# Optimization experiments

Hardware: AMD Instinct MI355X
Metric: run time of the kernel (lower is better)

Reference implementation:

```python
import jax, jax.numpy as jnp
import numpy as np

DIM = 1024
HEADS = 16
HEAD_DIM = DIM // HEADS


def rotate_half(x):
    x1, x2 = jnp.split(x, 2, axis=-1)
    return jnp.concatenate((-x2, x1), axis=-1)


def rope_tables(T, D, dtype=jnp.float32):
    inv_freq = 1.0 / (10000.0 ** (jnp.arange(0, D, 2, dtype=jnp.float32) / D))
    t = jnp.arange(T, dtype=jnp.float32)
    freqs = jnp.einsum('i,j->ij', t, inv_freq)  # [T, D/2]
    emb = jnp.concatenate((freqs, freqs), axis=-1)  # [T, D]
    return emb.astype(dtype), jnp.cos(emb).astype(dtype), jnp.sin(emb).astype(dtype)


def setup_inputs() -> dict:
    key = jax.random.key(0)
    kx, kq, kk, kv, ko = jax.random.split(key, 5)
    B, T = 2, 4096
    scale = 1.0 / np.sqrt(DIM)
    x = jax.random.normal(kx, (B, T, DIM), dtype=jnp.float32)
    wq = jax.random.normal(kq, (DIM, DIM), dtype=jnp.float32) * scale
    wk = jax.random.normal(kk, (DIM, DIM), dtype=jnp.float32) * scale
    wv = jax.random.normal(kv, (DIM, DIM), dtype=jnp.float32) * scale
    wo = jax.random.normal(ko, (DIM, DIM), dtype=jnp.float32) * scale
    return {"x": x, "wq": wq, "wk": wk, "wv": wv, "wo": wo}


def reference(x, wq, wk, wv, wo):
    B, T, C = x.shape
    H, D = HEADS, HEAD_DIM
    # projections; nn.Linear applies x @ W^T
    q = (x @ wq.T).reshape(B, T, H, D).transpose(0, 2, 1, 3)  # [B,H,T,D]
    k = (x @ wk.T).reshape(B, T, H, D).transpose(0, 2, 1, 3)
    v = (x @ wv.T).reshape(B, T, H, D).transpose(0, 2, 1, 3)
    _, cos, sin = rope_tables(T, D, x.dtype)
    cos = cos[None, None]  # [1,1,T,D]
    sin = sin[None, None]
    q = q * cos + rotate_half(q) * sin
    k = k * cos + rotate_half(k) * sin
    scores = jnp.einsum('bhtd,bhsd->bhts', q, k) / jnp.sqrt(jnp.asarray(D, x.dtype))
    attn = jax.nn.softmax(scores, axis=-1)
    out = jnp.einsum('bhts,bhsd->bhtd', attn, v)
    out = out.transpose(0, 2, 1, 3).reshape(B, T, C)
    return out @ wo.T
```

## Files before the change

kernel.cpp:

```cpp
#include <hip/hip_runtime.h>
#include <hip/hip_bf16.h>
#include <math.h>


typedef __attribute__((ext_vector_type(8))) short short8;
typedef __attribute__((ext_vector_type(4))) short short4v;
typedef __attribute__((ext_vector_type(4))) float floatx4;

using bf16 = __hip_bfloat16;

static constexpr int T_ = 4096;
static constexpr int C_ = 1024;
static constexpr int M_ = 8192;
static constexpr float QSCALE = 0.125f * 1.44269504088896340736f;

#if __has_builtin(__builtin_amdgcn_mfma_f32_16x16x16bf16_1k)
#define USE_K16 1
#else
#define USE_K16 0
#endif

#if __has_builtin(__builtin_amdgcn_exp2f)
#define EXP2 __builtin_amdgcn_exp2f
#else
#define EXP2 exp2f
#endif

__device__ __forceinline__ floatx4 mfma16(short8 a, short8 b, floatx4 c) {
    return __builtin_amdgcn_mfma_f32_16x16x32_bf16(a, b, c, 0, 0, 0);
}
#if USE_K16
__device__ __forceinline__ floatx4 mfma_k16(short4v a, short4v b, floatx4 c) {
    return __builtin_amdgcn_mfma_f32_16x16x16bf16_1k(a, b, c, 0, 0, 0);
}
#endif

__device__ __forceinline__ short8 ld8(const bf16* p) {
    return *reinterpret_cast<const short8*>(p);
}
__device__ __forceinline__ short4v ld4(const bf16* p) {
    return *reinterpret_cast<const short4v*>(p);
}
__device__ __forceinline__ void st8(bf16* p, short8 v) {
    *reinterpret_cast<short8*>(p) = v;
}
__device__ __forceinline__ unsigned short f2bf(float x) {
    bf16 h = __float2bfloat16(x);
    return reinterpret_cast<unsigned short&>(h);
}

__device__ __forceinline__ int pack2bf(float a, float b, unsigned sel) {
    const unsigned ua = __float_as_uint(a) + 0x8000u;
    const unsigned ub = __float_as_uint(b) + 0x8000u;
    int r;
    asm("v_perm_b32 %0, %1, %2, %3" : "=v"(r) : "v"(ub), "v"(ua), "s"(sel));
    return r;
}
__device__ __forceinline__ short4v i2s4(int lo, int hi) {
    union { int2 i; short4v s; } u;
    u.i.x = lo; u.i.y = hi;
    return u.s;
}
__device__ __forceinline__ short8 i2s8(int a, int b, int c, int d) {
    union { int4 i; short8 s; } u;
    u.i.x = a; u.i.y = b; u.i.z = c; u.i.w = d;
    return u.s;
}

__device__ __forceinline__ void cp16(const bf16* g, bf16* l) {
    __builtin_amdgcn_global_load_lds(
        (const __attribute__((address_space(1))) void*)g,
        (__attribute__((address_space(3))) void*)l, 16, 0, 0);
}

__global__ __launch_bounds__(256)
void prep_kernel(const float* __restrict__ x,
                 const float* __restrict__ wq, const float* __restrict__ wk,
                 const float* __restrict__ wv, const float* __restrict__ wo,
                 bf16* __restrict__ xb, bf16* __restrict__ wqb,
                 float2* __restrict__ CS) {
    const int blk = blockIdx.x;
    if (blk < 6144) {
        const float* in;
        bf16* out;
        int i;
        if (blk < 4096) {
            i = blk * 256 + threadIdx.x;
            in = x; out = xb;
        } else {
            i = (blk - 4096) * 256 + threadIdx.x;
            const int seg = i >> 17;
            const int off = i & 131071;
            in = (seg == 0) ? wq : (seg == 1) ? wk : (seg == 2) ? wv : wo;
            out = wqb + (size_t)i * 8 - (size_t)off * 8;
            i = off;
        }
        const float4* p = reinterpret_cast<const float4*>(in) + (size_t)i * 2;
        const float4 a = p[0];
        const float4 b = p[1];
        short8 v;
        v[0] = (short)f2bf(a.x); v[1] = (short)f2bf(a.y);
        v[2] = (short)f2bf(a.z); v[3] = (short)f2bf(a.w);
        v[4] = (short)f2bf(b.x); v[5] = (short)f2bf(b.y);
        v[6] = (short)f2bf(b.z); v[7] = (short)f2bf(b.w);
        *(reinterpret_cast<short8*>(out) + i) = v;
    } else {
        const int i = (blk - 6144) * 256 + threadIdx.x;
        const int t = i >> 5;
        const int j = i & 31;
        const float inv_freq = expf(-(float)j * 0.28782313662425575f);
        float s, c;
        sincosf((float)t * inv_freq, &s, &c);
        CS[i] = make_float2(c, s);
    }
}

#define GEMM_PROLOGUE(Ab, Wb)                                                 \
    _Pragma("unroll")                                                         \
    for (int j = 0; j < 2; ++j) {                                             \
        const int row = srow + j * 64;                                        \
        cp16((Ab) + (size_t)row * C_ + scol, &Als[0][(j * 256 + tid) * 8]);   \
        cp16((Wb) + (size_t)row * C_ + scol, &Bls[0][(j * 256 + tid) * 8]);   \
    }                                                                         \
    _Pragma("unroll")                                                         \
    for (int j = 0; j < 2; ++j) {                                             \
        const int row = srow + j * 64;                                        \
        cp16((Ab) + (size_t)row * C_ + 32 + scol, &Als[1][(j * 256 + tid) * 8]); \
        cp16((Wb) + (size_t)row * C_ + 32 + scol, &Bls[1][(j * 256 + tid) * 8]); \
    }

#define KSTEP(Ab, Wb, KK, BUF, LB, DOISSUE, VMN)                              \
    do {                                                                      \
        asm volatile("s_waitcnt vmcnt(" VMN ")" ::: "memory");                \
        __builtin_amdgcn_sched_barrier(0);                                    \
        __builtin_amdgcn_s_barrier();                                         \
        __builtin_amdgcn_sched_barrier(0);                                    \
        short8 a[4], b[4];                                                    \
        _Pragma("unroll")                                                     \
        for (int i = 0; i < 4; ++i)                                           \
            a[i] = ld8(&Als[BUF][(wr + i * 16 + lr) * 32 + quad * 8]);        \
        _Pragma("unroll")                                                     \
        for (int j = 0; j < 4; ++j)                                           \
            b[j] = ld8(&Bls[BUF][(wc + j * 16 + lr) * 32 + quad * 8]);        \
        if (DOISSUE) {                                                        \
            _Pragma("unroll")                                                 \
            for (int j = 0; j < 2; ++j) {                                     \
                const int row = srow + j * 64;                                \
                cp16((Ab) + (size_t)row * C_ + (KK) + 64 + scol,              \
                     &Als[LB][(j * 256 + tid) * 8]);                          \
                cp16((Wb) + (size_t)row * C_ + (KK) + 64 + scol,              \
                     &Bls[LB][(j * 256 + tid) * 8]);                          \
            }                                                                 \
        }                                                                     \
        _Pragma("unroll")                                                     \
        for (int i = 0; i < 4; ++i)                                           \
            _Pragma("unroll")                                                 \
            for (int j = 0; j < 4; ++j)                                       \
                acc[i][j] = mfma16(a[i], b[j], acc[i][j]);                    \
    } while (0)

#define GEMM_MAINLOOP(Ab, Wb)                                                 \
    GEMM_PROLOGUE(Ab, Wb)                                                     \
    for (int kk = 0; kk < 960; kk += 96) {                                    \
        KSTEP(Ab, Wb, kk,      0, 2, 1, "4");                                 \
        KSTEP(Ab, Wb, kk + 32, 1, 0, 1, "4");                                 \
        KSTEP(Ab, Wb, kk + 64, 2, 1, 1, "4");                                 \
    }                                                                         \
    KSTEP(Ab, Wb, 960, 0, 2, 0, "4");                                         \
    KSTEP(Ab, Wb, 992, 1, 0, 0, "0");

__global__ __launch_bounds__(256)
void gemm128_kernel(const bf16* __restrict__ A, const bf16* __restrict__ W,
                    void* __restrict__ out, int mode, int ntile, int cpx) {
    const int orig = blockIdx.x;
    const int swz  = (orig & 7) * cpx + (orig >> 3);
    const int m0   = (swz / ntile) * 128;
    const int n0   = (swz % ntile) * 128;
    const int tid  = threadIdx.x;
    const int lane = tid & 63;
    const int wave = tid >> 6;
    const int quad = lane >> 4;
    const int lr   = lane & 15;
    const int wr   = (wave >> 1) * 64;
    const int wc   = (wave & 1) * 64;

    __shared__ __align__(16) bf16 Als[3][128 * 32];
    __shared__ __align__(16) bf16 Bls[3][128 * 32];

    const int srow = tid >> 2;
    const int scol = (tid & 3) * 8;

    floatx4 acc[4][4];
#pragma unroll
    for (int i = 0; i < 4; ++i)
#pragma unroll
        for (int j = 0; j < 4; ++j) acc[i][j] = floatx4{0.f, 0.f, 0.f, 0.f};

    const bf16* Ab = A + (size_t)m0 * C_;
    const bf16* Wb = W + (size_t)n0 * C_;

    GEMM_MAINLOOP(Ab, Wb)

    if (mode == 0) {
        bf16* ob = (bf16*)out;
#pragma unroll
        for (int j = 0; j < 4; ++j) {
            const int col = n0 + wc + j * 16 + lr;
#pragma unroll
            for (int i = 0; i < 4; ++i)
#pragma unroll
                for (int r = 0; r < 4; ++r) {
                    const int m = m0 + wr + i * 16 + quad * 4 + r;
                    ob[(size_t)m * C_ + col] = __float2bfloat16(acc[i][j][r]);
                }
        }
    } else {
        float* of = (float*)out;
#pragma unroll
        for (int j = 0; j < 4; ++j) {
            const int col = n0 + wc + j * 16 + lr;
#pragma unroll
            for (int i = 0; i < 4; ++i)
#pragma unroll
                for (int r = 0; r < 4; ++r) {
                    const int m = m0 + wr + i * 16 + quad * 4 + r;
                    of[(size_t)m * C_ + col] = acc[i][j][r];
                }
        }
    }
}

__global__ __launch_bounds__(256)
void gemm_qkv_kernel(const bf16* __restrict__ A, const bf16* __restrict__ W,
                     bf16* __restrict__ Qbase, const float2* __restrict__ CS) {
    const int orig = blockIdx.x;
    const int swz  = (orig & 7) * 192 + (orig >> 3);
    const int m0   = (swz / 24) * 128;
    const int n0g  = (swz % 24) * 128;
    const int tid  = threadIdx.x;
    const int lane = tid & 63;
    const int wave = tid >> 6;
    const int quad = lane >> 4;
    const int lr   = lane & 15;
    const int wr   = (wave >> 1) * 64;
    const int wc   = (wave & 1) * 64;

    __shared__ __align__(16) bf16 Als[3][128 * 32];
    __shared__ __align__(16) bf16 Bls[3][128 * 32];

    const int srow = tid >> 2;
    const int scol = (tid & 3) * 8;

    floatx4 acc[4][4];
#pragma unroll
    for (int i = 0; i < 4; ++i)
#pragma unroll
        for (int j = 0; j < 4; ++j) acc[i][j] = floatx4{0.f, 0.f, 0.f, 0.f};

    const bf16* Ab = A + (size_t)m0 * C_;
    const bf16* Wb = W + (size_t)n0g * C_;

    GEMM_MAINLOOP(Ab, Wb)

    const int seg = n0g >> 10;
    const int n0  = n0g & 1023;
    if (seg < 2) {
        bf16* ob = Qbase + (size_t)seg * M_ * C_;
        const float scale = (seg == 0) ? QSCALE : 1.0f;
        const int tb = (m0 & 4095) + wr + quad * 4;
#pragma unroll
        for (int j = 0; j < 2; ++j) {
            const int col  = n0 + wc + j * 16 + lr;
            const int jcol = j * 16 + lr;
#pragma unroll
            for (int i = 0; i < 4; ++i) {
#pragma unroll
                for (int r = 0; r < 4; ++r) {
                    const int t = tb + i * 16 + r;
                    const float2 cs = CS[t * 32 + jcol];
                    const float q1 = acc[i][j][r];
                    const float q2 = acc[i][j + 2][r];
                    const int m = m0 + wr + i * 16 + quad * 4 + r;
                    ob[(size_t)m * C_ + col] =
                        __float2bfloat16((q1 * cs.x - q2 * cs.y) * scale);
                    ob[(size_t)m * C_ + col + 32] =
                        __float2bfloat16((q2 * cs.x + q1 * cs.y) * scale);
                }
            }
        }
    } else {
        unsigned short* ob = (unsigned short*)(Qbase + (size_t)2 * M_ * C_);
        const int b2 = m0 >> 12;
#pragma unroll
        for (int j = 0; j < 4; ++j) {
            const int n = n0 + wc + j * 16 + lr;
            const int h = n >> 6;
            const int d = n & 63;
#pragma unroll
            for (int i = 0; i < 4; ++i) {
                const int t0 = (m0 & 4095) + wr + i * 16 + quad * 4;
                ushort4 v;
                v.x = f2bf(acc[i][j][0]); v.y = f2bf(acc[i][j][1]);
                v.z = f2bf(acc[i][j][2]); v.w = f2bf(acc[i][j][3]);
                size_t idx = ((size_t)((b2 * 16 + h) * 64 + d)) * T_ + t0;
                *reinterpret_cast<ushort4*>(ob + idx) = v;
            }
        }
    }
}

__global__ __launch_bounds__(256)
void attn_kernel(const bf16* __restrict__ Q, const bf16* __restrict__ K,
                 const bf16* __restrict__ Vt, bf16* __restrict__ AO) {
    const int tid  = threadIdx.x;
    const int lane = tid & 63;
    const int wave = tid >> 6;
    const int quad = lane >> 4;
    const int lr   = lane & 15;
    const int bh   = blockIdx.y;
    const int b    = bh >> 4;
    const int h    = bh & 15;
    const int q0   = blockIdx.x * 128 + wave * 32;

    const bf16* Qb = Q + (size_t)b * T_ * C_ + h * 64;
    const bf16* Kb = K + (size_t)b * T_ * C_ + h * 64;
    const bf16* Vb = Vt + (size_t)bh * 64 * T_;

#if USE_K16
    __shared__ __align__(16) bf16 Kls[2][64 * 64];
    __shared__ __align__(16) bf16 Vls[2][64 * 64];

    const int srow  = tid >> 3;
    const int sc    = tid & 7;
    const int sphys = (sc ^ (srow & 7)) * 8;
    const int soff0 = srow * 64 + sphys;
    const int soff1 = (srow + 32) * 64 + sphys;

    const unsigned psel = 0x07060302u;
    const floatx4 FZ = {0.f, 0.f, 0.f, 0.f};
    const int one2 = 0x3F803F80;
    const short8 VONE = i2s8(one2, one2, one2, one2);

    short8 aq[2][2];
#pragma unroll
    for (int t = 0; t < 2; ++t) {
        aq[t][0] = ld8(Qb + (size_t)(q0 + t * 16 + lr) * C_ + quad * 8);
        aq[t][1] = ld8(Qb + (size_t)(q0 + t * 16 + lr) * C_ + 32 + quad * 8);
    }

    floatx4 O[2][4];
#pragma unroll
    for (int t = 0; t < 2; ++t)
#pragma unroll
        for (int dt = 0; dt < 4; ++dt) O[t][dt] = floatx4{0.f, 0.f, 0.f, 0.f};
    floatx4 Osum[2] = {{0.f, 0.f, 0.f, 0.f}, {0.f, 0.f, 0.f, 0.f}};

    const int lr7    = lr & 7;
    const int kchunk = (quad ^ lr7) * 8;
    const int vsub   = (quad & 1) * 4;
    const int vbq    = quad >> 1;
    const int kel0   = lr * 64 + kchunk;
    const int kel1   = kel0 ^ 32;
    int velk[4];
#pragma unroll
    for (int kk = 0; kk < 4; ++kk)
        velk[kk] = lr * 64 + (((2 * kk + vbq) ^ lr7) * 8) + vsub;

    short8 kr0, kr1, vr0, vr1;
#define LOAD_STAGE(kv0)                                              \
    do {                                                             \
        kr0 = ld8(Kb + (size_t)((kv0) + srow) * C_ + sc * 8);        \
        kr1 = ld8(Kb + (size_t)((kv0) + srow + 32) * C_ + sc * 8);   \
        vr0 = ld8(Vb + (size_t)srow * T_ + (kv0) + sc * 8);          \
        vr1 = ld8(Vb + (size_t)(srow + 32) * T_ + (kv0) + sc * 8);   \
    } while (0)
#define STORE_STAGE(p)                                               \
    do {                                                             \
        st8(&Kls[p][soff0], kr0);                                    \
        st8(&Kls[p][soff1], kr1);                                    \
        st8(&Vls[p][soff0], vr0);                                    \
        st8(&Vls[p][soff1], vr1);                                    \
    } while (0)

#define BAR()                                                        \
    do {                                                             \
        asm volatile("s_waitcnt lgkmcnt(0)" ::: "memory");           \
        __builtin_amdgcn_s_barrier();                                \
    } while (0)

#define COMPUTE(P)                                                            \
    do {                                                                      \
        const bf16* Ks = Kls[P];                                              \
        const bf16* Vs = Vls[P];                                              \
        int prlo[2][4], prhi[2][4];                                           \
        _Pragma("unroll")                                                     \
        for (int kk = 0; kk < 4; ++kk) {                                      \
            const short8 kf0 = ld8(Ks + kk * 1024 + kel0);                    \
            const short8 kf1 = ld8(Ks + kk * 1024 + kel1);                    \
            floatx4 s0 = mfma16(kf0, aq[0][0], FZ);                           \
            s0 = mfma16(kf1, aq[0][1], s0);                                   \
            floatx4 s1 = mfma16(kf0, aq[1][0], FZ);                           \
            s1 = mfma16(kf1, aq[1][1], s1);                                   \
            const float e0 = EXP2(s0[0]), e1 = EXP2(s0[1]);                   \
            const float e2 = EXP2(s0[2]), e3 = EXP2(s0[3]);                   \
            prlo[0][kk] = pack2bf(e0, e1, psel);                              \
            prhi[0][kk] = pack2bf(e2, e3, psel);                              \
            const float f0 = EXP2(s1[0]), f1 = EXP2(s1[1]);                   \
            const float f2 = EXP2(s1[2]), f3 = EXP2(s1[3]);                   \
            prlo[1][kk] = pack2bf(f0, f1, psel);                              \
            prhi[1][kk] = pack2bf(f2, f3, psel);                              \
        }                                                                     \
        \
        Osum[0] = mfma16(i2s8(prlo[0][0], prhi[0][0], prlo[0][1], prhi[0][1]),\
                         VONE, Osum[0]);                                      \
        Osum[0] = mfma16(i2s8(prlo[0][2], prhi[0][2], prlo[0][3], prhi[0][3]),\
                         VONE, Osum[0]);                                      \
        Osum[1] = mfma16(i2s8(prlo[1][0], prhi[1][0], prlo[1][1], prhi[1][1]),\
                         VONE, Osum[1]);                                      \
        Osum[1] = mfma16(i2s8(prlo[1][2], prhi[1][2], prlo[1][3], prhi[1][3]),\
                         VONE, Osum[1]);                                      \
        __builtin_amdgcn_s_setprio(1);                                        \
        _Pragma("unroll")                                                     \
        for (int dt = 0; dt < 4; ++dt) {                                      \
            _Pragma("unroll")                                                 \
            for (int kk = 0; kk < 4; ++kk) {                                  \
                const short4v vf = ld4(Vs + dt * 1024 + velk[kk]);            \
                O[0][dt] = mfma_k16(i2s4(prlo[0][kk], prhi[0][kk]), vf, O[0][dt]); \
                O[1][dt] = mfma_k16(i2s4(prlo[1][kk], prhi[1][kk]), vf, O[1][dt]); \
            }                                                                 \
        }                                                                     \
        __builtin_amdgcn_s_setprio(0);                                        \
    } while (0)

    LOAD_STAGE(0);
    STORE_STAGE(0);
    LOAD_STAGE(64);
    BAR();

    constexpr int NS = T_ / 64;
    for (int s = 0; s < NS; s += 2) {
        if (s + 1 < NS) STORE_STAGE(1);
        if (s + 2 < NS) LOAD_STAGE((s + 2) * 64);
        COMPUTE(0);
        BAR();
        if (s + 2 < NS) STORE_STAGE(0);
        if (s + 3 < NS) LOAD_STAGE((s + 3) * 64);
        COMPUTE(1);
        BAR();
    }

#pragma unroll
    for (int t = 0; t < 2; ++t) {
#pragma unroll
        for (int r = 0; r < 4; ++r) {
            const float inv = 1.0f / fmaxf(Osum[t][r], 1e-30f);
            const size_t row =
                (size_t)(b * T_ + q0 + t * 16 + quad * 4 + r) * C_ + h * 64;
            AO[row + 0  + lr] = __float2bfloat16(O[t][0][r] * inv);
            AO[row + 16 + lr] = __float2bfloat16(O[t][1][r] * inv);
            AO[row + 32 + lr] = __float2bfloat16(O[t][2][r] * inv);
            AO[row + 48 + lr] = __float2bfloat16(O[t][3][r] * inv);
        }
    }
#undef LOAD_STAGE
#undef STORE_STAGE
#undef COMPUTE
#undef BAR
#else
    __shared__ __align__(16) unsigned short Pbuf[4][512];
    unsigned short* Pw = Pbuf[wave];
    for (int half = 0; half < 2; ++half) {
        const int qh = q0 + half * 16;
        const short8 aq0 = ld8(Qb + (size_t)(qh + lr) * C_ + quad * 8);
        const short8 aq1 = ld8(Qb + (size_t)(qh + lr) * C_ + 32 + quad * 8);
        floatx4 O0 = {0,0,0,0}, O1 = {0,0,0,0}, O2 = {0,0,0,0}, O3 = {0,0,0,0};
        float lrun[4] = {0.f, 0.f, 0.f, 0.f};
        for (int kv = 0; kv < T_; kv += 32) {
            floatx4 S0 = {0,0,0,0}, S1 = {0,0,0,0};
            const bf16* k0 = Kb + (size_t)(kv + lr) * C_ + quad * 8;
            const bf16* k1 = Kb + (size_t)(kv + 16 + lr) * C_ + quad * 8;
            S0 = mfma16(aq0, ld8(k0), S0);
            S0 = mfma16(aq1, ld8(k0 + 32), S0);
            S1 = mfma16(aq0, ld8(k1), S1);
            S1 = mfma16(aq1, ld8(k1 + 32), S1);
#pragma unroll
            for (int r = 0; r < 4; ++r) {
                const float e0 = exp2f(S0[r]);
                const float e1 = exp2f(S1[r]);
                lrun[r] += e0 + e1;
                const int row = quad * 4 + r;
                Pw[row * 32 + lr]      = f2bf(e0);
                Pw[row * 32 + 16 + lr] = f2bf(e1);
            }
            __syncthreads();
            const short8 ap = *reinterpret_cast<const short8*>(Pw + lr * 32 + quad * 8);
            O0 = mfma16(ap, ld8(Vb + (size_t)(lr)      * T_ + kv + quad * 8), O0);
            O1 = mfma16(ap, ld8(Vb + (size_t)(16 + lr) * T_ + kv + quad * 8), O1);
            O2 = mfma16(ap, ld8(Vb + (size_t)(32 + lr) * T_ + kv + quad * 8), O2);
            O3 = mfma16(ap, ld8(Vb + (size_t)(48 + lr) * T_ + kv + quad * 8), O3);
            __syncthreads();
        }
#pragma unroll
        for (int r = 0; r < 4; ++r) {
            float l = lrun[r];
            l += __shfl_xor(l, 1); l += __shfl_xor(l, 2);
            l += __shfl_xor(l, 4); l += __shfl_xor(l, 8);
            const float inv = 1.0f / fmaxf(l, 1e-30f);
            const size_t row = (size_t)(b * T_ + qh + quad * 4 + r) * C_ + h * 64;
            AO[row + 0  + lr] = __float2bfloat16(O0[r] * inv);
            AO[row + 16 + lr] = __float2bfloat16(O1[r] * inv);
            AO[row + 32 + lr] = __float2bfloat16(O2[r] * inv);
            AO[row + 48 + lr] = __float2bfloat16(O3[r] * inv);
        }
    }
#endif
}

extern "C" void kernel_launch(void* const* d_in, const int* in_sizes, int n_in,
                              void* d_out, int out_size, void* d_ws, size_t ws_size,
                              hipStream_t stream) {
    const float* x  = (const float*)d_in[0];
    const float* wq = (const float*)d_in[1];
    const float* wk = (const float*)d_in[2];
    const float* wv = (const float*)d_in[3];
    const float* wo = (const float*)d_in[4];
    float* out = (float*)d_out;

    bf16* xb  = (bf16*)d_ws;
    bf16* wqb = xb  + (size_t)M_ * C_;
    bf16* wkb = wqb + (size_t)C_ * C_;
    bf16* wvb = wkb + (size_t)C_ * C_;
    bf16* wob = wvb + (size_t)C_ * C_;
    bf16* Q   = wob + (size_t)C_ * C_;
    bf16* K   = Q   + (size_t)M_ * C_;
    bf16* Vt  = K   + (size_t)M_ * C_;
    float2* CS = (float2*)(Vt + (size_t)M_ * C_);
    bf16* AO  = xb;

    prep_kernel<<<6656, 256, 0, stream>>>(x, wq, wk, wv, wo, xb, wqb, CS);

    gemm_qkv_kernel<<<1536, 256, 0, stream>>>(xb, wqb, Q, CS);

    attn_kernel<<<dim3(T_ / 128, 32), 256, 0, stream>>>(Q, K, Vt, AO);

    gemm128_kernel<<<512, 256, 0, stream>>>(AO, wob, out, 2, 8, 64);
}
```

Measured before the change: 371.2 us.

## Enlarge GEMM block tile to 256x128 with 512 threads

Both the QKV projection GEMM and the output GEMM move from 128x128 tiles with 4 waves to 256x128 tiles with 8 waves. Each stage now loads two A rows and one B row per thread, and the vmcnt wait is adjusted to match. The goal is to reuse each staged W tile across twice as many rows, which cuts global traffic and the number of blocks. In exchange LDS per block grows to about 72KB, and the output GEMM launches only 256 blocks, which may leave the device underfilled.

```diff
diff --git a/kernel.cpp b/kernel.cpp
--- a/kernel.cpp
+++ b/kernel.cpp
@@ -115,19 +115,14 @@
     }
 }
 
-#define GEMM_PROLOGUE(Ab, Wb)                                                 \
-    _Pragma("unroll")                                                         \
-    for (int j = 0; j < 2; ++j) {                                             \
-        const int row = srow + j * 64;                                        \
-        cp16((Ab) + (size_t)row * C_ + scol, &Als[0][(j * 256 + tid) * 8]);   \
-        cp16((Wb) + (size_t)row * C_ + scol, &Bls[0][(j * 256 + tid) * 8]);   \
-    }                                                                         \
-    _Pragma("unroll")                                                         \
-    for (int j = 0; j < 2; ++j) {                                             \
-        const int row = srow + j * 64;                                        \
-        cp16((Ab) + (size_t)row * C_ + 32 + scol, &Als[1][(j * 256 + tid) * 8]); \
-        cp16((Wb) + (size_t)row * C_ + 32 + scol, &Bls[1][(j * 256 + tid) * 8]); \
-    }
+#define GEMM_STAGE(Ab, Wb, KK, BUF)                                           \
+    do {                                                                      \
+        _Pragma("unroll")                                                     \
+        for (int j = 0; j < 2; ++j)                                           \
+            cp16((Ab) + (size_t)(srow + j * 128) * C_ + (KK) + scol,          \
+                 &Als[BUF][(j * 512 + tid) * 8]);                             \
+        cp16((Wb) + (size_t)srow * C_ + (KK) + scol, &Bls[BUF][tid * 8]);     \
+    } while (0)
 
 #define KSTEP(Ab, Wb, KK, BUF, LB, DOISSUE, VMN)                              \
     do {                                                                      \
@@ -142,16 +137,7 @@
         _Pragma("unroll")                                                     \
         for (int j = 0; j < 4; ++j)                                           \
             b[j] = ld8(&Bls[BUF][(wc + j * 16 + lr) * 32 + quad * 8]);        \
-        if (DOISSUE) {                                                        \
-            _Pragma("unroll")                                                 \
-            for (int j = 0; j < 2; ++j) {                                     \
-                const int row = srow + j * 64;                                \
-                cp16((Ab) + (size_t)row * C_ + (KK) + 64 + scol,              \
-                     &Als[LB][(j * 256 + tid) * 8]);                          \
-                cp16((Wb) + (size_t)row * C_ + (KK) + 64 + scol,              \
-                     &Bls[LB][(j * 256 + tid) * 8]);                          \
-            }                                                                 \
-        }                                                                     \
+        if (DOISSUE) GEMM_STAGE(Ab, Wb, (KK) + 64, LB);                       \
         _Pragma("unroll")                                                     \
         for (int i = 0; i < 4; ++i)                                           \
             _Pragma("unroll")                                                 \
@@ -160,21 +146,22 @@
     } while (0)
 
 #define GEMM_MAINLOOP(Ab, Wb)                                                 \
-    GEMM_PROLOGUE(Ab, Wb)                                                     \
+    GEMM_STAGE(Ab, Wb, 0, 0);                                                 \
+    GEMM_STAGE(Ab, Wb, 32, 1);                                                \
     for (int kk = 0; kk < 960; kk += 96) {                                    \
-        KSTEP(Ab, Wb, kk,      0, 2, 1, "4");                                 \
-        KSTEP(Ab, Wb, kk + 32, 1, 0, 1, "4");                                 \
-        KSTEP(Ab, Wb, kk + 64, 2, 1, 1, "4");                                 \
+        KSTEP(Ab, Wb, kk,      0, 2, 1, "3");                                 \
+        KSTEP(Ab, Wb, kk + 32, 1, 0, 1, "3");                                 \
+        KSTEP(Ab, Wb, kk + 64, 2, 1, 1, "3");                                 \
     }                                                                         \
-    KSTEP(Ab, Wb, 960, 0, 2, 0, "4");                                         \
+    KSTEP(Ab, Wb, 960, 0, 2, 0, "3");                                         \
     KSTEP(Ab, Wb, 992, 1, 0, 0, "0");
 
-__global__ __launch_bounds__(256)
+__global__ __launch_bounds__(512, 4)
 void gemm128_kernel(const bf16* __restrict__ A, const bf16* __restrict__ W,
                     void* __restrict__ out, int mode, int ntile, int cpx) {
     const int orig = blockIdx.x;
     const int swz  = (orig & 7) * cpx + (orig >> 3);
-    const int m0   = (swz / ntile) * 128;
+    const int m0   = (swz / ntile) * 256;
     const int n0   = (swz % ntile) * 128;
     const int tid  = threadIdx.x;
     const int lane = tid & 63;
@@ -184,7 +171,7 @@
     const int wr   = (wave >> 1) * 64;
     const int wc   = (wave & 1) * 64;
 
-    __shared__ __align__(16) bf16 Als[3][128 * 32];
+    __shared__ __align__(16) bf16 Als[3][256 * 32];
     __shared__ __align__(16) bf16 Bls[3][128 * 32];
 
     const int srow = tid >> 2;
@@ -230,12 +217,12 @@
     }
 }
 
-__global__ __launch_bounds__(256)
+__global__ __launch_bounds__(512, 4)
 void gemm_qkv_kernel(const bf16* __restrict__ A, const bf16* __restrict__ W,
                      bf16* __restrict__ Qbase, const float2* __restrict__ CS) {
     const int orig = blockIdx.x;
-    const int swz  = (orig & 7) * 192 + (orig >> 3);
-    const int m0   = (swz / 24) * 128;
+    const int swz  = (orig & 7) * 96 + (orig >> 3);
+    const int m0   = (swz / 24) * 256;
     const int n0g  = (swz % 24) * 128;
     const int tid  = threadIdx.x;
     const int lane = tid & 63;
@@ -245,7 +232,7 @@
     const int wr   = (wave >> 1) * 64;
     const int wc   = (wave & 1) * 64;
 
-    __shared__ __align__(16) bf16 Als[3][128 * 32];
+    __shared__ __align__(16) bf16 Als[3][256 * 32];
     __shared__ __align__(16) bf16 Bls[3][128 * 32];
 
     const int srow = tid >> 2;
@@ -539,9 +526,9 @@
 
     prep_kernel<<<6656, 256, 0, stream>>>(x, wq, wk, wv, wo, xb, wqb, CS);
 
-    gemm_qkv_kernel<<<1536, 256, 0, stream>>>(xb, wqb, Q, CS);
+    gemm_qkv_kernel<<<768, 512, 0, stream>>>(xb, wqb, Q, CS);
 
     attn_kernel<<<dim3(T_ / 128, 32), 256, 0, stream>>>(Q, K, Vt, AO);
 
-    gemm128_kernel<<<512, 256, 0, stream>>>(AO, wob, out, 2, 8, 64);
-}
+    gemm128_kernel<<<256, 512, 0, stream>>>(AO, wob, out, 2, 8, 32);
+}
```

New measurement: 354.5 us. 4.5% less time.
